# Performance work log

Measured on AMD Instinct MI355X. Metric: run time of the kernel, lower is better.

Reference implementation:

```python
import jax, jax.numpy as jnp
import numpy as np
from jax import lax

B, T = 1048576, 30

def setup_inputs() -> dict:
    key = jax.random.key(0)
    k = jax.random.split(key, 5)
    return {
        "x": jax.random.normal(k[0], (B, T, 1), dtype=jnp.float32),
        "W1": jax.random.normal(k[1], (T, 2, 20), dtype=jnp.float32) * 0.5,
        "b1": jax.random.normal(k[2], (T, 20), dtype=jnp.float32) * 0.1,
        "W2": jax.random.normal(k[3], (T, 20, 1), dtype=jnp.float32) * 0.5,
        "b2": jax.random.normal(k[4], (T, 1), dtype=jnp.float32) * 0.1,
    }

def reference(x, W1, b1, W2, b2):
    # x: [B, T, 1]; per-timestep MLP with recurrent concat of previous output.
    xt = jnp.transpose(x, (1, 0, 2))  # [T, B, 1]
    h0 = jnp.zeros((x.shape[0], 1), dtype=x.dtype)  # output_0

    def step(prev_out, inp):
        xi, w1, bb1, w2, bb2 = inp  # xi: [B,1], w1: [2,20], w2: [20,1]
        ih = jnp.concatenate([xi, prev_out], axis=1)       # [B, 2]
        h = jax.nn.relu(ih @ w1 + bb1)                     # [B, 20]
        o = jnp.tanh(h @ w2 + bb2)                         # [B, 1]
        return o, o

    _, outs = lax.scan(step, h0, (xt, W1, b1, W2, b2))  # outs: [T, B, 1]
    return jnp.transpose(outs, (1, 0, 2))  # [B, T, 1]
```

## Files before the change

### kernel.cpp

```cpp
#include <hip/hip_runtime.h>


#define TS  30
#define HID 20
#define THR 256
#define EPB 512
#define ROW 514

typedef float f2 __attribute__((ext_vector_type(2)));

__device__ __forceinline__ float fast_tanh(float y) {
    float e = __expf(2.0f * y);
    return 1.0f - 2.0f * __builtin_amdgcn_rcpf(e + 1.0f);
}

__global__ __launch_bounds__(256) void repack_w(
        const float* __restrict__ W1, const float* __restrict__ b1,
        const float* __restrict__ W2, const float* __restrict__ b2,
        float4* __restrict__ wp) {
    for (int i = threadIdx.x; i < TS * 21; i += 256) {
        const int t = i / 21;
        const int j = i - t * 21;
        float4 v;
        if (j < HID) v = make_float4(W1[t * 40 + j], W1[t * 40 + 20 + j],
                                     b1[t * 20 + j], W2[t * 20 + j]);
        else         v = make_float4(b2[t], 0.f, 0.f, 0.f);
        wp[i] = v;
    }
}

__global__ __launch_bounds__(256) void rnn2(
        const float* __restrict__ x,
        const float4* __restrict__ wp,
        float* __restrict__ out) {
    __shared__ float tile[TS * ROW];
    const int tid = threadIdx.x;
    const size_t gbase = (size_t)blockIdx.x * (EPB * TS);

    const float4* xg = reinterpret_cast<const float4*>(x + gbase);
#pragma unroll
    for (int i = 0; i < 15; ++i) {
        float4 v = xg[i * THR + tid];
        const unsigned fo = (unsigned)(i * THR + tid) * 4u;
        const float* vp = reinterpret_cast<const float*>(&v);
#pragma unroll
        for (int k = 0; k < 4; ++k) {
            const unsigned f = fo + k;
            const unsigned e = (f * 34953u) >> 20;
            const unsigned t = f - e * 30u;
            tile[t * ROW + e] = vp[k];
        }
    }
    __syncthreads();

    f2 o = {0.f, 0.f};
    const int e0 = 2 * tid;
#pragma unroll 1
    for (int t = 0; t < TS; ++t) {
        const float4* wr = wp + t * 21;
        const f2 xv = *reinterpret_cast<const f2*>(&tile[t * ROW + e0]);
        const float bb = wr[20].x;
        f2 acc = {bb, bb};
#pragma unroll
        for (int j = 0; j < HID; ++j) {
            const float4 w = wr[j];
            f2 h = xv * w.x + o * w.y + w.z;
            h.x = __builtin_fmaxf(h.x, 0.f);
            h.y = __builtin_fmaxf(h.y, 0.f);
            acc += h * w.w;
        }
        o.x = fast_tanh(acc.x);
        o.y = fast_tanh(acc.y);
        *reinterpret_cast<f2*>(&tile[t * ROW + e0]) = o;
    }
    __syncthreads();

    float4* og = reinterpret_cast<float4*>(out + gbase);
#pragma unroll
    for (int i = 0; i < 15; ++i) {
        const unsigned fo = (unsigned)(i * THR + tid) * 4u;
        float4 v;
        float* vp = reinterpret_cast<float*>(&v);
#pragma unroll
        for (int k = 0; k < 4; ++k) {
            const unsigned f = fo + k;
            const unsigned e = (f * 34953u) >> 20;
            const unsigned t = f - e * 30u;
            vp[k] = tile[t * ROW + e];
        }
        og[i * THR + tid] = v;
    }
}

extern "C" void kernel_launch(void* const* d_in, const int* in_sizes, int n_in,
                              void* d_out, int out_size, void* d_ws, size_t ws_size,
                              hipStream_t stream) {
    const float* x  = (const float*)d_in[0];
    const float* W1 = (const float*)d_in[1];
    const float* b1 = (const float*)d_in[2];
    const float* W2 = (const float*)d_in[3];
    const float* b2 = (const float*)d_in[4];
    float* out = (float*)d_out;
    float4* wp = (float4*)d_ws;

    repack_w<<<1, 256, 0, stream>>>(W1, b1, W2, b2, wp);

    const int B = 1048576;
    const int grid = B / EPB;
    rnn2<<<grid, 256, 0, stream>>>(x, wp, out);
}
```

Measured before the change: 265.9 us.

## Process one batch element per thread with smaller tiles for higher occupancy

```diff
diff --git a/kernel.cpp b/kernel.cpp
--- a/kernel.cpp
+++ b/kernel.cpp
@@ -4,10 +4,8 @@
 #define TS  30
 #define HID 20
 #define THR 256
-#define EPB 512
-#define ROW 514
-
-typedef float f2 __attribute__((ext_vector_type(2)));
+#define EPB 256
+#define ROW 257
 
 __device__ __forceinline__ float fast_tanh(float y) {
     float e = __expf(2.0f * y);
@@ -29,7 +27,7 @@
     }
 }
 
-__global__ __launch_bounds__(256) void rnn2(
+__global__ __launch_bounds__(256, 5) void rnn3(
         const float* __restrict__ x,
         const float4* __restrict__ wp,
         float* __restrict__ out) {
@@ -37,57 +35,52 @@
     const int tid = threadIdx.x;
     const size_t gbase = (size_t)blockIdx.x * (EPB * TS);
 
-    const float4* xg = reinterpret_cast<const float4*>(x + gbase);
+    const float2* xg = reinterpret_cast<const float2*>(x + gbase);
 #pragma unroll
     for (int i = 0; i < 15; ++i) {
-        float4 v = xg[i * THR + tid];
-        const unsigned fo = (unsigned)(i * THR + tid) * 4u;
-        const float* vp = reinterpret_cast<const float*>(&v);
-#pragma unroll
-        for (int k = 0; k < 4; ++k) {
-            const unsigned f = fo + k;
-            const unsigned e = (f * 34953u) >> 20;
-            const unsigned t = f - e * 30u;
-            tile[t * ROW + e] = vp[k];
-        }
+        const float2 v = xg[i * THR + tid];
+        const unsigned f0 = (unsigned)(i * THR + tid) * 2u;
+        const unsigned e0 = (f0 * 34953u) >> 20;
+        const unsigned t0 = f0 - e0 * 30u;
+        tile[t0 * ROW + e0] = v.x;
+        const unsigned f1 = f0 + 1u;
+        const unsigned e1 = (f1 * 34953u) >> 20;
+        const unsigned t1 = f1 - e1 * 30u;
+        tile[t1 * ROW + e1] = v.y;
     }
     __syncthreads();
 
-    f2 o = {0.f, 0.f};
-    const int e0 = 2 * tid;
+    float o = 0.f;
 #pragma unroll 1
     for (int t = 0; t < TS; ++t) {
         const float4* wr = wp + t * 21;
-        const f2 xv = *reinterpret_cast<const f2*>(&tile[t * ROW + e0]);
-        const float bb = wr[20].x;
-        f2 acc = {bb, bb};
+        const float xv = tile[t * ROW + tid];
+        float acc = wr[20].x;
 #pragma unroll
         for (int j = 0; j < HID; ++j) {
             const float4 w = wr[j];
-            f2 h = xv * w.x + o * w.y + w.z;
-            h.x = __builtin_fmaxf(h.x, 0.f);
-            h.y = __builtin_fmaxf(h.y, 0.f);
-            acc += h * w.w;
+            float h = __builtin_fmaf(o, w.y, w.z);
+            h = __builtin_fmaf(xv, w.x, h);
+            h = __builtin_fmaxf(h, 0.f);
+            acc = __builtin_fmaf(h, w.w, acc);
         }
-        o.x = fast_tanh(acc.x);
-        o.y = fast_tanh(acc.y);
-        *reinterpret_cast<f2*>(&tile[t * ROW + e0]) = o;
+        o = fast_tanh(acc);
+        tile[t * ROW + tid] = o;
     }
     __syncthreads();
 
-    float4* og = reinterpret_cast<float4*>(out + gbase);
+    float2* og = reinterpret_cast<float2*>(out + gbase);
 #pragma unroll
     for (int i = 0; i < 15; ++i) {
-        const unsigned fo = (unsigned)(i * THR + tid) * 4u;
-        float4 v;
-        float* vp = reinterpret_cast<float*>(&v);
-#pragma unroll
-        for (int k = 0; k < 4; ++k) {
-            const unsigned f = fo + k;
-            const unsigned e = (f * 34953u) >> 20;
-            const unsigned t = f - e * 30u;
-            vp[k] = tile[t * ROW + e];
-        }
+        const unsigned f0 = (unsigned)(i * THR + tid) * 2u;
+        const unsigned e0 = (f0 * 34953u) >> 20;
+        const unsigned t0 = f0 - e0 * 30u;
+        const unsigned f1 = f0 + 1u;
+        const unsigned e1 = (f1 * 34953u) >> 20;
+        const unsigned t1 = f1 - e1 * 30u;
+        float2 v;
+        v.x = tile[t0 * ROW + e0];
+        v.y = tile[t1 * ROW + e1];
         og[i * THR + tid] = v;
     }
 }
@@ -107,5 +100,5 @@
 
     const int B = 1048576;
     const int grid = B / EPB;
-    rnn2<<<grid, 256, 0, stream>>>(x, wp, out);
+    rnn3<<<grid, 256, 0, stream>>>(x, wp, out);
 }
```

Measured after the change: 259.3 us. 2.5% less time.

## Process timesteps in three chunks with smaller swizzled LDS tile

Applied to the files above, without the earlier changes.

```diff
diff --git a/kernel.cpp b/kernel.cpp
--- a/kernel.cpp
+++ b/kernel.cpp
@@ -1,11 +1,12 @@
 #include <hip/hip_runtime.h>
 
 
-#define TS  30
-#define HID 20
-#define THR 256
-#define EPB 512
-#define ROW 514
+#define TS   30
+#define CH   10
+#define NCH  3
+#define THR  256
+#define EPB  512
+#define ROW  512
 
 typedef float f2 __attribute__((ext_vector_type(2)));
 
@@ -22,73 +23,75 @@
         const int t = i / 21;
         const int j = i - t * 21;
         float4 v;
-        if (j < HID) v = make_float4(W1[t * 40 + j], W1[t * 40 + 20 + j],
-                                     b1[t * 20 + j], W2[t * 20 + j]);
-        else         v = make_float4(b2[t], 0.f, 0.f, 0.f);
+        if (j < 20) v = make_float4(W1[t * 40 + j], W1[t * 40 + 20 + j],
+                                    b1[t * 20 + j], W2[t * 20 + j]);
+        else        v = make_float4(b2[t], 0.f, 0.f, 0.f);
         wp[i] = v;
     }
 }
 
-__global__ __launch_bounds__(256) void rnn2(
+__global__ __launch_bounds__(256, 8) void rnn4(
         const float* __restrict__ x,
         const float4* __restrict__ wp,
         float* __restrict__ out) {
-    __shared__ float tile[TS * ROW];
+    __shared__ float tile[CH * ROW];
     const int tid = threadIdx.x;
-    const size_t gbase = (size_t)blockIdx.x * (EPB * TS);
+    const size_t gb2 = (size_t)blockIdx.x * (EPB * TS / 2);
+    const float2* xg = reinterpret_cast<const float2*>(x);
+    float2* og = reinterpret_cast<float2*>(out);
 
-    const float4* xg = reinterpret_cast<const float4*>(x + gbase);
+    const int e0 = 2 * tid;
+    f2 o = {0.f, 0.f};
+
+#pragma unroll 1
+    for (int c = 0; c < NCH; ++c) {
 #pragma unroll
-    for (int i = 0; i < 15; ++i) {
-        float4 v = xg[i * THR + tid];
-        const unsigned fo = (unsigned)(i * THR + tid) * 4u;
-        const float* vp = reinterpret_cast<const float*>(&v);
+        for (int i = 0; i < CH; ++i) {
+            const unsigned p = (unsigned)(i * THR + tid);
+            const unsigned e = (p * 52429u) >> 18;
+            const unsigned q = p - e * 5u;
+            const float2 v = xg[gb2 + e * 15u + (unsigned)c * 5u + q];
+            const unsigned tt0 = 2u * q;
+            tile[tt0 * ROW + (e ^ (2u * tt0))]             = v.x;
+            tile[(tt0 + 1u) * ROW + (e ^ (2u * tt0 + 2u))] = v.y;
+        }
+        __syncthreads();
+
+#pragma unroll 1
+        for (int tt = 0; tt < CH; ++tt) {
+            const int t = c * CH + tt;
+            const float4* wr = wp + t * 21;
+            const unsigned idx = (unsigned)tt * ROW +
+                                 ((unsigned)e0 ^ (2u * (unsigned)tt));
+            const f2 xv = *reinterpret_cast<const f2*>(&tile[idx]);
+            const float bb = wr[20].x;
+            f2 acc = {bb, bb};
 #pragma unroll
-        for (int k = 0; k < 4; ++k) {
-            const unsigned f = fo + k;
-            const unsigned e = (f * 34953u) >> 20;
-            const unsigned t = f - e * 30u;
-            tile[t * ROW + e] = vp[k];
+            for (int j = 0; j < 20; ++j) {
+                const float4 w = wr[j];
+                f2 h = xv * w.x + o * w.y + w.z;
+                h.x = __builtin_fmaxf(h.x, 0.f);
+                h.y = __builtin_fmaxf(h.y, 0.f);
+                acc += h * w.w;
+            }
+            o.x = fast_tanh(acc.x);
+            o.y = fast_tanh(acc.y);
+            *reinterpret_cast<f2*>(&tile[idx]) = o;
         }
-    }
-    __syncthreads();
+        __syncthreads();
 
-    f2 o = {0.f, 0.f};
-    const int e0 = 2 * tid;
-#pragma unroll 1
-    for (int t = 0; t < TS; ++t) {
-        const float4* wr = wp + t * 21;
-        const f2 xv = *reinterpret_cast<const f2*>(&tile[t * ROW + e0]);
-        const float bb = wr[20].x;
-        f2 acc = {bb, bb};
 #pragma unroll
-        for (int j = 0; j < HID; ++j) {
-            const float4 w = wr[j];
-            f2 h = xv * w.x + o * w.y + w.z;
-            h.x = __builtin_fmaxf(h.x, 0.f);
-            h.y = __builtin_fmaxf(h.y, 0.f);
-            acc += h * w.w;
+        for (int i = 0; i < CH; ++i) {
+            const unsigned p = (unsigned)(i * THR + tid);
+            const unsigned e = (p * 52429u) >> 18;
+            const unsigned q = p - e * 5u;
+            const unsigned tt0 = 2u * q;
+            float2 v;
+            v.x = tile[tt0 * ROW + (e ^ (2u * tt0))];
+            v.y = tile[(tt0 + 1u) * ROW + (e ^ (2u * tt0 + 2u))];
+            og[gb2 + e * 15u + (unsigned)c * 5u + q] = v;
         }
-        o.x = fast_tanh(acc.x);
-        o.y = fast_tanh(acc.y);
-        *reinterpret_cast<f2*>(&tile[t * ROW + e0]) = o;
-    }
-    __syncthreads();
-
-    float4* og = reinterpret_cast<float4*>(out + gbase);
-#pragma unroll
-    for (int i = 0; i < 15; ++i) {
-        const unsigned fo = (unsigned)(i * THR + tid) * 4u;
-        float4 v;
-        float* vp = reinterpret_cast<float*>(&v);
-#pragma unroll
-        for (int k = 0; k < 4; ++k) {
-            const unsigned f = fo + k;
-            const unsigned e = (f * 34953u) >> 20;
-            const unsigned t = f - e * 30u;
-            vp[k] = tile[t * ROW + e];
-        }
-        og[i * THR + tid] = v;
+        __syncthreads();
     }
 }
 
@@ -107,5 +110,5 @@
 
     const int B = 1048576;
     const int grid = B / EPB;
-    rnn2<<<grid, 256, 0, stream>>>(x, wp, out);
+    rnn4<<<grid, 256, 0, stream>>>(x, wp, out);
 }
```

Measured after the change: 396.7 us. +49.2%, slower.

## Keep per-thread sequences in registers instead of shared-memory transpose tile

Applied to the files above, without the earlier changes.

```diff
diff --git a/kernel.cpp b/kernel.cpp
--- a/kernel.cpp
+++ b/kernel.cpp
@@ -4,8 +4,6 @@
 #define TS  30
 #define HID 20
 #define THR 256
-#define EPB 512
-#define ROW 514
 
 typedef float f2 __attribute__((ext_vector_type(2)));
 
@@ -17,78 +15,72 @@
 __global__ __launch_bounds__(256) void repack_w(
         const float* __restrict__ W1, const float* __restrict__ b1,
         const float* __restrict__ W2, const float* __restrict__ b2,
-        float4* __restrict__ wp) {
+        f2* __restrict__ wp2) {
     for (int i = threadIdx.x; i < TS * 21; i += 256) {
         const int t = i / 21;
         const int j = i - t * 21;
-        float4 v;
-        if (j < HID) v = make_float4(W1[t * 40 + j], W1[t * 40 + 20 + j],
-                                     b1[t * 20 + j], W2[t * 20 + j]);
-        else         v = make_float4(b2[t], 0.f, 0.f, 0.f);
-        wp[i] = v;
+        f2 a, b, c, d;
+        if (j < HID) {
+            const float wx = W1[t * 40 + j];
+            const float wh = W1[t * 40 + 20 + j];
+            const float bb = b1[t * 20 + j];
+            const float w2 = W2[t * 20 + j];
+            a = (f2){wx, wx}; b = (f2){wh, wh};
+            c = (f2){bb, bb}; d = (f2){w2, w2};
+        } else {
+            const float bb2 = b2[t];
+            a = (f2){bb2, bb2}; b = (f2){0.f, 0.f};
+            c = (f2){0.f, 0.f}; d = (f2){0.f, 0.f};
+        }
+        f2* o = wp2 + (size_t)i * 4;
+        o[0] = a; o[1] = b; o[2] = c; o[3] = d;
     }
 }
 
-__global__ __launch_bounds__(256) void rnn2(
+__global__ __launch_bounds__(256, 4) void rnn5(
         const float* __restrict__ x,
-        const float4* __restrict__ wp,
+        const f2* __restrict__ wp2,
         float* __restrict__ out) {
-    __shared__ float tile[TS * ROW];
     const int tid = threadIdx.x;
-    const size_t gbase = (size_t)blockIdx.x * (EPB * TS);
+    const size_t base4 = ((size_t)blockIdx.x * THR + tid) * 15u;
+    const float4* xg = reinterpret_cast<const float4*>(x);
 
-    const float4* xg = reinterpret_cast<const float4*>(x + gbase);
+    float rf[60];
 #pragma unroll
     for (int i = 0; i < 15; ++i) {
-        float4 v = xg[i * THR + tid];
-        const unsigned fo = (unsigned)(i * THR + tid) * 4u;
-        const float* vp = reinterpret_cast<const float*>(&v);
-#pragma unroll
-        for (int k = 0; k < 4; ++k) {
-            const unsigned f = fo + k;
-            const unsigned e = (f * 34953u) >> 20;
-            const unsigned t = f - e * 30u;
-            tile[t * ROW + e] = vp[k];
-        }
+        const float4 v = xg[base4 + i];
+        rf[4 * i + 0] = v.x; rf[4 * i + 1] = v.y;
+        rf[4 * i + 2] = v.z; rf[4 * i + 3] = v.w;
     }
-    __syncthreads();
 
     f2 o = {0.f, 0.f};
-    const int e0 = 2 * tid;
-#pragma unroll 1
+#pragma unroll
     for (int t = 0; t < TS; ++t) {
-        const float4* wr = wp + t * 21;
-        const f2 xv = *reinterpret_cast<const f2*>(&tile[t * ROW + e0]);
-        const float bb = wr[20].x;
-        f2 acc = {bb, bb};
+        const f2* wr = wp2 + t * 84;
+        const f2 xv = {rf[t], rf[30 + t]};
+        f2 acc = wr[80];
 #pragma unroll
         for (int j = 0; j < HID; ++j) {
-            const float4 w = wr[j];
-            f2 h = xv * w.x + o * w.y + w.z;
+            const f2 wx = wr[4 * j + 0];
+            const f2 wh = wr[4 * j + 1];
+            const f2 bb = wr[4 * j + 2];
+            const f2 w2 = wr[4 * j + 3];
+            f2 h = xv * wx + o * wh + bb;
             h.x = __builtin_fmaxf(h.x, 0.f);
             h.y = __builtin_fmaxf(h.y, 0.f);
-            acc += h * w.w;
+            acc += h * w2;
         }
         o.x = fast_tanh(acc.x);
         o.y = fast_tanh(acc.y);
-        *reinterpret_cast<f2*>(&tile[t * ROW + e0]) = o;
+        rf[t] = o.x; rf[30 + t] = o.y;
     }
-    __syncthreads();
 
-    float4* og = reinterpret_cast<float4*>(out + gbase);
+    float4* og = reinterpret_cast<float4*>(out);
 #pragma unroll
     for (int i = 0; i < 15; ++i) {
-        const unsigned fo = (unsigned)(i * THR + tid) * 4u;
-        float4 v;
-        float* vp = reinterpret_cast<float*>(&v);
-#pragma unroll
-        for (int k = 0; k < 4; ++k) {
-            const unsigned f = fo + k;
-            const unsigned e = (f * 34953u) >> 20;
-            const unsigned t = f - e * 30u;
-            vp[k] = tile[t * ROW + e];
-        }
-        og[i * THR + tid] = v;
+        const float4 v = make_float4(rf[4 * i + 0], rf[4 * i + 1],
+                                     rf[4 * i + 2], rf[4 * i + 3]);
+        og[base4 + i] = v;
     }
 }
 
@@ -101,11 +93,11 @@
     const float* W2 = (const float*)d_in[3];
     const float* b2 = (const float*)d_in[4];
     float* out = (float*)d_out;
-    float4* wp = (float4*)d_ws;
+    f2* wp2 = (f2*)d_ws;
 
-    repack_w<<<1, 256, 0, stream>>>(W1, b1, W2, b2, wp);
+    repack_w<<<1, 256, 0, stream>>>(W1, b1, W2, b2, wp2);
 
     const int B = 1048576;
-    const int grid = B / EPB;
-    rnn2<<<grid, 256, 0, stream>>>(x, wp, out);
+    const int grid = B / (2 * THR);
+    rnn5<<<grid, THR, 0, stream>>>(x, wp2, out);
 }
```

After: 360.0 us. 1.35x slower.
